# Performance work log

Measured on AMD Instinct MI355X. Metric: run time of the kernel, lower is better.

The kernel has to match this reference:

```python
import jax, jax.numpy as jnp
import numpy as np

B, L, D, H, S = 2, 2048, 1024, 16, 4
Dh = D // H
EPS = 1e-5


def setup_inputs() -> dict:
    key = jax.random.key(0)
    ks = jax.random.split(key, 12)
    sc = 0.02
    w = lambda k, shape: (jax.random.normal(k, shape, jnp.float32) * sc)
    M = 2 * S  # number of MHA blocks / dense linears
    inp = {
        "response": jax.random.normal(ks[0], (B, L, D), jnp.float32),
        "mask": jnp.broadcast_to(jnp.tril(jnp.ones((L, L), bool)), (B, L, L)),
        "Wq": w(ks[1], (M, D, D)), "bq": w(ks[2], (M, D)),
        "Wk": w(ks[3], (M, D, D)), "bk": w(ks[4], (M, D)),
        "Wv": w(ks[5], (M, D, D)), "bv": w(ks[6], (M, D)),
        "Wo": w(ks[7], (M, D, D)), "bo": w(ks[8], (M, D)),
        "Wd": w(ks[9], (M, D, D)), "bd": w(ks[10], (M, D)),
    }
    return inp


def _ln(x):
    # fresh LayerNorm(d) with default weight=1, bias=0, eps=1e-5
    m = jnp.mean(x, axis=-1, keepdims=True)
    v = jnp.mean((x - m) ** 2, axis=-1, keepdims=True)
    return (x - m) * jax.lax.rsqrt(v + EPS)


def _linear(x, W, b):
    # torch Linear: x @ W.T + b
    return jnp.einsum('bld,od->blo', x, W) + b


def _mha(x, i, mask, Wq, bq, Wk, bk, Wv, bv, Wo, bo):
    # self-attention: q = k = v = x
    split = lambda y: y.reshape(B, L, H, Dh).transpose(0, 2, 1, 3)  # (B,H,L,Dh)
    q = split(_linear(x, Wq[i], bq[i]))
    k = split(_linear(x, Wk[i], bk[i]))
    v = split(_linear(x, Wv[i], bv[i]))
    scores = jnp.einsum('bhqd,bhkd->bhqk', q, k) / jnp.sqrt(jnp.float32(Dh))
    if mask is not None:
        scores = jnp.where(mask[:, None, :, :], scores, -jnp.inf)
    p = jnp.nan_to_num(jax.nn.softmax(scores, axis=-1))
    o = jnp.einsum('bhqk,bhkd->bhqd', p, v).transpose(0, 2, 1, 3).reshape(B, L, D)
    return _linear(o, Wo[i], bo[i])


def reference(response, mask, Wq, bq, Wk, bk, Wv, bv, Wo, bo, Wd, bd):
    x = response
    for i in range(S):
        # masked self-attention + residual + LN
        x = _ln(x + _mha(x, 2 * i, mask, Wq, bq, Wk, bk, Wv, bv, Wo, bo))
        # encoder-attention sublayer (encMem is None -> unmasked self-attention)
        x = _ln(x + _mha(x, 2 * i + 1, None, Wq, bq, Wk, bk, Wv, bv, Wo, bo))
        # dense: linear[2i](LeakyReLU(linear[2i+1](x)))
        h = jax.nn.leaky_relu(_linear(x, Wd[2 * i + 1], bd[2 * i + 1]), negative_slope=0.01)
        h = _linear(h, Wd[2 * i], bd[2 * i])
        x = _ln(x + h)
    return x
```

## Files before the change

kernel.cpp:

```cpp
#include <hip/hip_runtime.h>
#include <stdint.h>
#include <stddef.h>

typedef __attribute__((ext_vector_type(8))) _Float16 f16x8;
typedef __attribute__((ext_vector_type(4))) _Float16 f16x4;
typedef __attribute__((ext_vector_type(4))) float    f32x4;

#define NB 2
#define NL 2048
#define ND 1024
#define NH 16
#define NROWS (NB*NL)

__device__ __forceinline__ void async16(void* lds, const void* g) {
  __builtin_amdgcn_global_load_lds(
      (const __attribute__((address_space(1))) void*)g,
      (__attribute__((address_space(3))) void*)lds, 16, 0, 0);
}

struct CvtArgs { const float* in[5]; _Float16* out[5]; };

__global__ __launch_bounds__(256) void cvt_all(CvtArgs a, int n4)
{
  const float* in  = a.in[blockIdx.z];
  _Float16*   out  = a.out[blockIdx.z];
  for (int i = blockIdx.x * blockDim.x + threadIdx.x; i < n4;
       i += gridDim.x * blockDim.x) {
    float4 v = ((const float4*)in)[i];
    f16x4 o = {(_Float16)v.x, (_Float16)v.y, (_Float16)v.z, (_Float16)v.w};
    ((f16x4*)out)[i] = o;
  }
}

__global__ __launch_bounds__(256) void init_x(
    const float* __restrict__ r, float* __restrict__ x,
    _Float16* __restrict__ xh, int n4)
{
  for (int i = blockIdx.x * blockDim.x + threadIdx.x; i < n4;
       i += gridDim.x * blockDim.x) {
    float4 v = ((const float4*)r)[i];
    ((float4*)x)[i] = v;
    f16x4 o = {(_Float16)v.x, (_Float16)v.y, (_Float16)v.z, (_Float16)v.w};
    ((f16x4*)xh)[i] = o;
  }
}

struct GArgs {
  const _Float16* A;
  const _Float16* B[3];
  const float*    bias[3];
  void*           out[3];
  int             mode[3];
};

__global__ __launch_bounds__(256, 2) void gemm_bt(GArgs ga)
{
  __shared__ _Float16 As[2][128 * 64];
  __shared__ _Float16 Bs[2][128 * 64];
  const int tid = threadIdx.x;
  const int w = tid >> 6, l = tid & 63;
  const int ql = l & 15, g = l >> 4;
  const int widx = blockIdx.x >> 3;
  const _Float16* Bw  = ga.B[widx];
  const float*   bias = ga.bias[widx];
  void*          outp = ga.out[widx];
  const int      mode = ga.mode[widx];
  const int brow = blockIdx.y * 128;
  const int bcol = (blockIdx.x & 7) * 128;
  const int wm = w >> 1, wn = w & 1;
  f32x4 acc[4][4] = {};

  const int srow = w * 32 + (l >> 3);
  const int scol = ((l & 7) ^ (l >> 3)) << 3;
  const _Float16* Ag = ga.A + (size_t)(brow + srow) * ND + scol;
  const _Float16* Bg = Bw   + (size_t)(bcol + srow) * ND + scol;

#define STAGE(buf, k0_)                                                  \
  {                                                                      \
    _Float16* AsW = &As[buf][w * 2048];                                  \
    _Float16* BsW = &Bs[buf][w * 2048];                                  \
    _Pragma("unroll")                                                    \
    for (int i = 0; i < 4; ++i) {                                        \
      async16(AsW + i * 512, Ag + (size_t)i * 8 * ND + (k0_));           \
      async16(BsW + i * 512, Bg + (size_t)i * 8 * ND + (k0_));           \
    }                                                                    \
  }

  STAGE(0, 0);
  for (int k0 = 0; k0 < ND; k0 += 64) {
    const int cur = (k0 >> 6) & 1;
    if (k0 + 64 < ND) {
      STAGE(cur ^ 1, k0 + 64);
      asm volatile("s_waitcnt vmcnt(8)" ::: "memory");
    } else {
      asm volatile("s_waitcnt vmcnt(0)" ::: "memory");
    }
    __builtin_amdgcn_s_barrier();
#pragma unroll
    for (int ks = 0; ks < 64; ks += 32) {
      const int cx = (ks + g * 8) ^ ((ql & 7) << 3);
      f16x8 af[4], bf[4];
#pragma unroll
      for (int mi = 0; mi < 4; ++mi)
        af[mi] = *(const f16x8*)&As[cur][(wm * 64 + mi * 16 + ql) * 64 + cx];
#pragma unroll
      for (int nj = 0; nj < 4; ++nj)
        bf[nj] = *(const f16x8*)&Bs[cur][(wn * 64 + nj * 16 + ql) * 64 + cx];
#pragma unroll
      for (int mi = 0; mi < 4; ++mi)
#pragma unroll
        for (int nj = 0; nj < 4; ++nj)
          acc[mi][nj] = __builtin_amdgcn_mfma_f32_16x16x32_f16(
              af[mi], bf[nj], acc[mi][nj], 0, 0, 0);
    }
    asm volatile("s_waitcnt lgkmcnt(0)" ::: "memory");
    __builtin_amdgcn_s_barrier();
  }
#undef STAGE

  const int colb = bcol + wn * 64;
  const int rowb = brow + wm * 64 + g * 4;
  if (mode == 3) {
    _Float16* vt = (_Float16*)outp;
    const int bb = rowb >> 11;
#pragma unroll
    for (int nj = 0; nj < 4; ++nj) {
      const int col = colb + nj * 16 + ql;
      const float bv = bias[col];
      const int hh = col >> 6, d = col & 63;
      _Float16* vrow = vt + ((size_t)((bb * NH + hh) * 64 + d)) * NL;
#pragma unroll
      for (int mi = 0; mi < 4; ++mi) {
        const int krow = (rowb + mi * 16) & (NL - 1);
        f16x4 o;
#pragma unroll
        for (int r = 0; r < 4; ++r) o[r] = (_Float16)(acc[mi][nj][r] + bv);
        *(f16x4*)(vrow + krow) = o;
      }
    }
  } else {
    _Float16* oh = (_Float16*)outp;
#pragma unroll
    for (int nj = 0; nj < 4; ++nj) {
      const int col = colb + nj * 16 + ql;
      const float bv = bias[col];
#pragma unroll
      for (int mi = 0; mi < 4; ++mi) {
#pragma unroll
        for (int r = 0; r < 4; ++r) {
          float v = acc[mi][nj][r] + bv;
          if (mode == 2) v = v > 0.f ? v : 0.01f * v;
          oh[(size_t)(rowb + mi * 16 + r) * ND + col] = (_Float16)v;
        }
      }
    }
  }
}

template<bool CAUSAL>
__global__ __launch_bounds__(512) void attn_fwd(
    const _Float16* __restrict__ Q, const _Float16* __restrict__ K,
    const _Float16* __restrict__ Vt, _Float16* __restrict__ O)
{
  __shared__ _Float16 kv[2][2][64 * 64];
  __shared__ unsigned int pls[8][16 * 34];
  const int tid = threadIdx.x;
  const int w = tid >> 6, l = tid & 63;
  const int ql = l & 15, g = l >> 4;
  const int h = blockIdx.y, b = blockIdx.z;
  const int qt = (CAUSAL && b) ? (NL / 128 - 1 - blockIdx.x) : blockIdx.x;
  const int qrow = qt * 128 + w * 16 + ql;

  const _Float16* Qp = Q + (size_t)(b * NL + qrow) * ND + h * 64 + g * 8;
  const f16x8 bq0 = *(const f16x8*)Qp;
  const f16x8 bq1 = *(const f16x8*)(Qp + 32);

  const int srow = w * 8 + (l >> 3);
  const int scol = ((l & 7) ^ (l >> 3)) << 3;
  const _Float16* Kg = K  + ((size_t)(b * NL) + srow) * ND + h * 64 + scol;
  const _Float16* Vg = Vt + ((size_t)((b * NH + h) * 64 + srow)) * NL + scol;

  const int msk  = (ql & 7) << 3;
  const int offA = ql * 64 + ((     g * 8) ^ msk);
  const int offB = ql * 64 + ((32 + g * 8) ^ msk);

  unsigned int* pw = &pls[w][0];
  f32x4 ot[4] = {};
  float s_run = 0.f;
  const int ntiles = CAUSAL ? (qt * 2 + 2) : (NL / 64);
  const float SCL = 0.125f * 1.44269504089f;
  const float M2  = 4.0f * 1.44269504089f;

  async16(&kv[0][0][w * 512], Kg);
  async16(&kv[0][1][w * 512], Vg);

  for (int kt = 0; kt < ntiles; ++kt) {
    const int nb = kt & 1;
    const size_t nk0 = (size_t)((kt + 1 < ntiles) ? kt + 1 : kt) * 64;
    async16(&kv[nb ^ 1][0][w * 512], Kg + nk0 * ND);
    async16(&kv[nb ^ 1][1][w * 512], Vg + nk0);
    asm volatile("s_waitcnt vmcnt(2)" ::: "memory");
    __builtin_amdgcn_s_barrier();

    const _Float16* kb = &kv[nb][0][0];
    const _Float16* vb = &kv[nb][1][0];
    const int k0 = kt * 64;
    f32x4 st[4] = {};
#pragma unroll
    for (int sub = 0; sub < 4; ++sub) {
      const f16x8 a0 = *(const f16x8*)&kb[sub * 1024 + offA];
      const f16x8 a1 = *(const f16x8*)&kb[sub * 1024 + offB];
      st[sub] = __builtin_amdgcn_mfma_f32_16x16x32_f16(a0, bq0, st[sub], 0, 0, 0);
      st[sub] = __builtin_amdgcn_mfma_f32_16x16x32_f16(a1, bq1, st[sub], 0, 0, 0);
    }
    float ps = 0.f;
    float pv[16];
#pragma unroll
    for (int sub = 0; sub < 4; ++sub)
#pragma unroll
      for (int r = 0; r < 4; ++r) {
        float p = exp2f(__builtin_fmaf(st[sub][r], SCL, -M2));
        if (CAUSAL && (k0 + sub * 16 + g * 4 + r) > qrow) p = 0.f;
        pv[sub * 4 + r] = p;
        ps += p;
      }
#pragma unroll
    for (int sub = 0; sub < 4; ++sub) {
      uint2 uu;
      uu.x = __builtin_bit_cast(unsigned int,
                __builtin_amdgcn_cvt_pkrtz(pv[sub * 4 + 0], pv[sub * 4 + 1]));
      uu.y = __builtin_bit_cast(unsigned int,
                __builtin_amdgcn_cvt_pkrtz(pv[sub * 4 + 2], pv[sub * 4 + 3]));
      *(uint2*)&pw[(sub * 4 + g) * 34 + 2 * ql] = uu;
    }
    ps += __shfl_xor(ps, 16);
    ps += __shfl_xor(ps, 32);
    s_run += ps;

#pragma unroll
    for (int hh = 0; hh < 2; ++hh) {
      uint2 lo = *(const uint2*)&pw[(hh * 8 + 2 * g    ) * 34 + 2 * ql];
      uint2 hi = *(const uint2*)&pw[(hh * 8 + 2 * g + 1) * 34 + 2 * ql];
      uint4 ui; ui.x = lo.x; ui.y = lo.y; ui.z = hi.x; ui.w = hi.y;
      const f16x8 pf = __builtin_bit_cast(f16x8, ui);
      const int voff = hh ? offB : offA;
#pragma unroll
      for (int dt = 0; dt < 4; ++dt) {
        const f16x8 vf = *(const f16x8*)&vb[dt * 1024 + voff];
        ot[dt] = __builtin_amdgcn_mfma_f32_16x16x32_f16(vf, pf, ot[dt], 0, 0, 0);
      }
    }
    asm volatile("s_waitcnt lgkmcnt(0)" ::: "memory");
    __builtin_amdgcn_s_barrier();
  }

  const float inv = 1.f / s_run;
#pragma unroll
  for (int dt = 0; dt < 4; ++dt) {
    f16x4 o;
#pragma unroll
    for (int r = 0; r < 4; ++r) o[r] = (_Float16)(ot[dt][r] * inv);
    *(f16x4*)(O + (size_t)(b * NL + qrow) * ND + h * 64 + dt * 16 + g * 4) = o;
  }
}

__global__ __launch_bounds__(256) void resid_ln(
    const float* __restrict__ x, const _Float16* __restrict__ dlt,
    float* __restrict__ xo, _Float16* __restrict__ xh)
{
  const int row = blockIdx.x, tid = threadIdx.x;
  const float4 xv = ((const float4*)(x + (size_t)row * ND))[tid];
  const f16x4 dv = ((const f16x4*)(dlt + (size_t)row * ND))[tid];
  const float a = xv.x + (float)dv[0], b = xv.y + (float)dv[1];
  const float c = xv.z + (float)dv[2], d = xv.w + (float)dv[3];
  float s = a + b + c + d;
  float ss = a * a + b * b + c * c + d * d;
#pragma unroll
  for (int m = 1; m < 64; m <<= 1) {
    s  += __shfl_xor(s, m);
    ss += __shfl_xor(ss, m);
  }
  __shared__ float red[8];
  if ((tid & 63) == 0) { red[tid >> 6] = s; red[4 + (tid >> 6)] = ss; }
  __syncthreads();
  const float S  = red[0] + red[1] + red[2] + red[3];
  const float SS = red[4] + red[5] + red[6] + red[7];
  const float mean = S * (1.0f / ND);
  const float var  = SS * (1.0f / ND) - mean * mean;
  const float rstd = rsqrtf(fmaxf(var, 0.f) + 1e-5f);
  float4 y;
  y.x = (a - mean) * rstd; y.y = (b - mean) * rstd;
  y.z = (c - mean) * rstd; y.w = (d - mean) * rstd;
  ((float4*)(xo + (size_t)row * ND))[tid] = y;
  f16x4 yh = {(_Float16)y.x, (_Float16)y.y, (_Float16)y.z, (_Float16)y.w};
  ((f16x4*)(xh + (size_t)row * ND))[tid] = yh;
}

extern "C" void kernel_launch(void* const* d_in, const int* in_sizes, int n_in,
                              void* d_out, int out_size, void* d_ws, size_t ws_size,
                              hipStream_t stream)
{
  (void)in_sizes; (void)n_in; (void)out_size; (void)ws_size;
  const float* response = (const float*)d_in[0];
  const float* Wq = (const float*)d_in[2];
  const float* bq = (const float*)d_in[3];
  const float* Wk = (const float*)d_in[4];
  const float* bk = (const float*)d_in[5];
  const float* Wv = (const float*)d_in[6];
  const float* bv = (const float*)d_in[7];
  const float* Wo = (const float*)d_in[8];
  const float* bo = (const float*)d_in[9];
  const float* Wd = (const float*)d_in[10];
  const float* bd = (const float*)d_in[11];
  float* x = (float*)d_out;

  const size_t MB = 1024 * 1024;
  char* p = (char*)d_ws;
  _Float16* Wq_h = (_Float16*)(p + 0 * MB);
  _Float16* Wk_h = (_Float16*)(p + 16 * MB);
  _Float16* Wv_h = (_Float16*)(p + 32 * MB);
  _Float16* Wo_h = (_Float16*)(p + 48 * MB);
  _Float16* Wd_h = (_Float16*)(p + 64 * MB);
  _Float16* xh   = (_Float16*)(p + 80 * MB);
  _Float16* Qh   = (_Float16*)(p + 88 * MB);
  _Float16* Kh   = (_Float16*)(p + 96 * MB);
  _Float16* Vth  = (_Float16*)(p + 104 * MB);
  _Float16* Oh   = (_Float16*)(p + 112 * MB);
  _Float16* h1   = Qh;
  _Float16* tmp  = (_Float16*)(p + 96 * MB);

  const int wn4 = 8 * 1024 * 1024 / 4;
  CvtArgs ca = { { Wq, Wk, Wv, Wo, Wd }, { Wq_h, Wk_h, Wv_h, Wo_h, Wd_h } };
  cvt_all<<<dim3(256, 1, 5), 256, 0, stream>>>(ca, wn4);
  init_x<<<1024, 256, 0, stream>>>(response, x, xh, NROWS * ND / 4);

  const dim3 g3(24, NROWS / 128);
  const dim3 g1(8, NROWS / 128);
  const dim3 agrid(NL / 128, NH, NB);

  for (int i = 0; i < 4; ++i) {
    for (int sub = 0; sub < 2; ++sub) {
      const int m = 2 * i + sub;
      const size_t wo = (size_t)m * MB;
      const size_t bf = (size_t)m * 1024;
      GArgs qkv = { xh,
                    { Wq_h + wo, Wk_h + wo, Wv_h + wo },
                    { bq + bf, bk + bf, bv + bf },
                    { Qh, Kh, Vth }, { 0, 0, 3 } };
      gemm_bt<<<g3, 256, 0, stream>>>(qkv);
      if (sub == 0) attn_fwd<true ><<<agrid, 512, 0, stream>>>(Qh, Kh, Vth, Oh);
      else          attn_fwd<false><<<agrid, 512, 0, stream>>>(Qh, Kh, Vth, Oh);
      GArgs oprj = { Oh,
                     { Wo_h + wo, nullptr, nullptr },
                     { bo + bf, nullptr, nullptr },
                     { tmp, nullptr, nullptr }, { 0, 0, 0 } };
      gemm_bt<<<g1, 256, 0, stream>>>(oprj);
      resid_ln<<<NROWS, 256, 0, stream>>>(x, tmp, x, xh);
    }
    const size_t w1 = (size_t)(2 * i + 1) * MB, b1 = (size_t)(2 * i + 1) * 1024;
    const size_t w0 = (size_t)(2 * i) * MB,     b0 = (size_t)(2 * i) * 1024;
    GArgs f1 = { xh,
                 { Wd_h + w1, nullptr, nullptr },
                 { bd + b1, nullptr, nullptr },
                 { h1, nullptr, nullptr }, { 2, 0, 0 } };
    gemm_bt<<<g1, 256, 0, stream>>>(f1);
    GArgs f2 = { h1,
                 { Wd_h + w0, nullptr, nullptr },
                 { bd + b0, nullptr, nullptr },
                 { tmp, nullptr, nullptr }, { 0, 0, 0 } };
    gemm_bt<<<g1, 256, 0, stream>>>(f2);
    resid_ln<<<NROWS, 256, 0, stream>>>(x, tmp, x, xh);
  }
}
```

Baseline: 1.320 ms.

## Split-K the output and second FFN GEMMs; give attention waves two query fragments

The O-projection and second dense GEMM now split K into two halves across blockIdx.z and write fp16 partials to two buffers. The residual-LayerNorm kernel sums both partials, which doubles the block count for 1024-wide GEMMs that previously launched only 256 blocks. Separately, the attention kernel drops from 8 waves of 16 query rows to 4 waves of 32 rows each, so every K/V fragment loaded from LDS feeds two query tiles, with launch bounds set for three blocks per CU. The cost is extra partial-sum traffic, fp16 rounding of each partial, and more registers per attention wave.

```diff
diff --git a/kernel.cpp b/kernel.cpp
--- a/kernel.cpp
+++ b/kernel.cpp
@@ -51,6 +51,7 @@
   const float*    bias[3];
   void*           out[3];
   int             mode[3];
+  int             ksplit;
 };
 
 __global__ __launch_bounds__(256, 2) void gemm_bt(GArgs ga)
@@ -60,11 +61,15 @@
   const int tid = threadIdx.x;
   const int w = tid >> 6, l = tid & 63;
   const int ql = l & 15, g = l >> 4;
-  const int widx = blockIdx.x >> 3;
+  const int z = blockIdx.z;
+  const int widx = ga.ksplit ? 0 : (blockIdx.x >> 3);
   const _Float16* Bw  = ga.B[widx];
   const float*   bias = ga.bias[widx];
-  void*          outp = ga.out[widx];
+  void*          outp = ga.ksplit ? ga.out[z] : ga.out[widx];
   const int      mode = ga.mode[widx];
+  const int kbeg = ga.ksplit ? z * (ND / 2) : 0;
+  const int kend = ga.ksplit ? kbeg + ND / 2 : ND;
+  const bool dobias = (!ga.ksplit) || (z == 0);
   const int brow = blockIdx.y * 128;
   const int bcol = (blockIdx.x & 7) * 128;
   const int wm = w >> 1, wn = w & 1;
@@ -86,10 +91,10 @@
     }                                                                    \
   }
 
-  STAGE(0, 0);
-  for (int k0 = 0; k0 < ND; k0 += 64) {
-    const int cur = (k0 >> 6) & 1;
-    if (k0 + 64 < ND) {
+  STAGE(0, kbeg);
+  for (int k0 = kbeg; k0 < kend; k0 += 64) {
+    const int cur = ((k0 - kbeg) >> 6) & 1;
+    if (k0 + 64 < kend) {
       STAGE(cur ^ 1, k0 + 64);
       asm volatile("s_waitcnt vmcnt(8)" ::: "memory");
     } else {
@@ -143,7 +148,7 @@
 #pragma unroll
     for (int nj = 0; nj < 4; ++nj) {
       const int col = colb + nj * 16 + ql;
-      const float bv = bias[col];
+      const float bv = dobias ? bias[col] : 0.f;
 #pragma unroll
       for (int mi = 0; mi < 4; ++mi) {
 #pragma unroll
@@ -158,24 +163,29 @@
 }
 
 template<bool CAUSAL>
-__global__ __launch_bounds__(512) void attn_fwd(
+__global__ __launch_bounds__(256, 3) void attn_fwd(
     const _Float16* __restrict__ Q, const _Float16* __restrict__ K,
     const _Float16* __restrict__ Vt, _Float16* __restrict__ O)
 {
   __shared__ _Float16 kv[2][2][64 * 64];
-  __shared__ unsigned int pls[8][16 * 34];
+  __shared__ unsigned int pls[4][2][16 * 34];
   const int tid = threadIdx.x;
   const int w = tid >> 6, l = tid & 63;
   const int ql = l & 15, g = l >> 4;
   const int h = blockIdx.y, b = blockIdx.z;
-  const int qt = (CAUSAL && b) ? (NL / 128 - 1 - blockIdx.x) : blockIdx.x;
-  const int qrow = qt * 128 + w * 16 + ql;
-
-  const _Float16* Qp = Q + (size_t)(b * NL + qrow) * ND + h * 64 + g * 8;
-  const f16x8 bq0 = *(const f16x8*)Qp;
-  const f16x8 bq1 = *(const f16x8*)(Qp + 32);
-
-  const int srow = w * 8 + (l >> 3);
+  const int qt = (CAUSAL && b) ? (NL / 128 - 1 - (int)blockIdx.x) : blockIdx.x;
+
+  f16x8 bq[2][2];
+  int qrow[2];
+#pragma unroll
+  for (int f = 0; f < 2; ++f) {
+    qrow[f] = qt * 128 + w * 32 + f * 16 + ql;
+    const _Float16* Qp = Q + (size_t)(b * NL + qrow[f]) * ND + h * 64 + g * 8;
+    bq[f][0] = *(const f16x8*)Qp;
+    bq[f][1] = *(const f16x8*)(Qp + 32);
+  }
+
+  const int srow = w * 16 + (l >> 3);
   const int scol = ((l & 7) ^ (l >> 3)) << 3;
   const _Float16* Kg = K  + ((size_t)(b * NL) + srow) * ND + h * 64 + scol;
   const _Float16* Vg = Vt + ((size_t)((b * NH + h) * 64 + srow)) * NL + scol;
@@ -184,95 +194,114 @@
   const int offA = ql * 64 + ((     g * 8) ^ msk);
   const int offB = ql * 64 + ((32 + g * 8) ^ msk);
 
-  unsigned int* pw = &pls[w][0];
-  f32x4 ot[4] = {};
-  float s_run = 0.f;
+  f32x4 ot[2][4] = {};
+  float s_run[2] = {0.f, 0.f};
   const int ntiles = CAUSAL ? (qt * 2 + 2) : (NL / 64);
   const float SCL = 0.125f * 1.44269504089f;
   const float M2  = 4.0f * 1.44269504089f;
 
-  async16(&kv[0][0][w * 512], Kg);
-  async16(&kv[0][1][w * 512], Vg);
+  async16(&kv[0][0][w * 1024      ], Kg);
+  async16(&kv[0][0][w * 1024 + 512], Kg + (size_t)8 * ND);
+  async16(&kv[0][1][w * 1024      ], Vg);
+  async16(&kv[0][1][w * 1024 + 512], Vg + (size_t)8 * NL);
 
   for (int kt = 0; kt < ntiles; ++kt) {
     const int nb = kt & 1;
     const size_t nk0 = (size_t)((kt + 1 < ntiles) ? kt + 1 : kt) * 64;
-    async16(&kv[nb ^ 1][0][w * 512], Kg + nk0 * ND);
-    async16(&kv[nb ^ 1][1][w * 512], Vg + nk0);
-    asm volatile("s_waitcnt vmcnt(2)" ::: "memory");
+    async16(&kv[nb ^ 1][0][w * 1024      ], Kg + nk0 * ND);
+    async16(&kv[nb ^ 1][0][w * 1024 + 512], Kg + nk0 * ND + (size_t)8 * ND);
+    async16(&kv[nb ^ 1][1][w * 1024      ], Vg + nk0);
+    async16(&kv[nb ^ 1][1][w * 1024 + 512], Vg + nk0 + (size_t)8 * NL);
+    asm volatile("s_waitcnt vmcnt(4)" ::: "memory");
     __builtin_amdgcn_s_barrier();
 
     const _Float16* kb = &kv[nb][0][0];
     const _Float16* vb = &kv[nb][1][0];
     const int k0 = kt * 64;
-    f32x4 st[4] = {};
-#pragma unroll
-    for (int sub = 0; sub < 4; ++sub) {
-      const f16x8 a0 = *(const f16x8*)&kb[sub * 1024 + offA];
-      const f16x8 a1 = *(const f16x8*)&kb[sub * 1024 + offB];
-      st[sub] = __builtin_amdgcn_mfma_f32_16x16x32_f16(a0, bq0, st[sub], 0, 0, 0);
-      st[sub] = __builtin_amdgcn_mfma_f32_16x16x32_f16(a1, bq1, st[sub], 0, 0, 0);
-    }
-    float ps = 0.f;
-    float pv[16];
-#pragma unroll
-    for (int sub = 0; sub < 4; ++sub)
-#pragma unroll
-      for (int r = 0; r < 4; ++r) {
-        float p = exp2f(__builtin_fmaf(st[sub][r], SCL, -M2));
-        if (CAUSAL && (k0 + sub * 16 + g * 4 + r) > qrow) p = 0.f;
-        pv[sub * 4 + r] = p;
-        ps += p;
-      }
-#pragma unroll
-    for (int sub = 0; sub < 4; ++sub) {
-      uint2 uu;
-      uu.x = __builtin_bit_cast(unsigned int,
-                __builtin_amdgcn_cvt_pkrtz(pv[sub * 4 + 0], pv[sub * 4 + 1]));
-      uu.y = __builtin_bit_cast(unsigned int,
-                __builtin_amdgcn_cvt_pkrtz(pv[sub * 4 + 2], pv[sub * 4 + 3]));
-      *(uint2*)&pw[(sub * 4 + g) * 34 + 2 * ql] = uu;
-    }
-    ps += __shfl_xor(ps, 16);
-    ps += __shfl_xor(ps, 32);
-    s_run += ps;
+
+#pragma unroll
+    for (int f = 0; f < 2; ++f) {
+      f32x4 st[4] = {};
+#pragma unroll
+      for (int sub = 0; sub < 4; ++sub) {
+        const f16x8 a0 = *(const f16x8*)&kb[sub * 1024 + offA];
+        const f16x8 a1 = *(const f16x8*)&kb[sub * 1024 + offB];
+        st[sub] = __builtin_amdgcn_mfma_f32_16x16x32_f16(a0, bq[f][0], st[sub], 0, 0, 0);
+        st[sub] = __builtin_amdgcn_mfma_f32_16x16x32_f16(a1, bq[f][1], st[sub], 0, 0, 0);
+      }
+      float ps = 0.f;
+      float pv[16];
+#pragma unroll
+      for (int sub = 0; sub < 4; ++sub)
+#pragma unroll
+        for (int r = 0; r < 4; ++r) {
+          float p = exp2f(__builtin_fmaf(st[sub][r], SCL, -M2));
+          if (CAUSAL && (k0 + sub * 16 + g * 4 + r) > qrow[f]) p = 0.f;
+          pv[sub * 4 + r] = p;
+          ps += p;
+        }
+#pragma unroll
+      for (int sub = 0; sub < 4; ++sub) {
+        uint2 uu;
+        uu.x = __builtin_bit_cast(unsigned int,
+                  __builtin_amdgcn_cvt_pkrtz(pv[sub * 4 + 0], pv[sub * 4 + 1]));
+        uu.y = __builtin_bit_cast(unsigned int,
+                  __builtin_amdgcn_cvt_pkrtz(pv[sub * 4 + 2], pv[sub * 4 + 3]));
+        *(uint2*)&pls[w][f][(sub * 4 + g) * 34 + 2 * ql] = uu;
+      }
+      ps += __shfl_xor(ps, 16);
+      ps += __shfl_xor(ps, 32);
+      s_run[f] += ps;
+    }
 
 #pragma unroll
     for (int hh = 0; hh < 2; ++hh) {
-      uint2 lo = *(const uint2*)&pw[(hh * 8 + 2 * g    ) * 34 + 2 * ql];
-      uint2 hi = *(const uint2*)&pw[(hh * 8 + 2 * g + 1) * 34 + 2 * ql];
-      uint4 ui; ui.x = lo.x; ui.y = lo.y; ui.z = hi.x; ui.w = hi.y;
-      const f16x8 pf = __builtin_bit_cast(f16x8, ui);
+      f16x8 pf[2];
+#pragma unroll
+      for (int f = 0; f < 2; ++f) {
+        uint2 lo = *(const uint2*)&pls[w][f][(hh * 8 + 2 * g    ) * 34 + 2 * ql];
+        uint2 hi = *(const uint2*)&pls[w][f][(hh * 8 + 2 * g + 1) * 34 + 2 * ql];
+        uint4 ui; ui.x = lo.x; ui.y = lo.y; ui.z = hi.x; ui.w = hi.y;
+        pf[f] = __builtin_bit_cast(f16x8, ui);
+      }
       const int voff = hh ? offB : offA;
 #pragma unroll
       for (int dt = 0; dt < 4; ++dt) {
         const f16x8 vf = *(const f16x8*)&vb[dt * 1024 + voff];
-        ot[dt] = __builtin_amdgcn_mfma_f32_16x16x32_f16(vf, pf, ot[dt], 0, 0, 0);
+        ot[0][dt] = __builtin_amdgcn_mfma_f32_16x16x32_f16(vf, pf[0], ot[0][dt], 0, 0, 0);
+        ot[1][dt] = __builtin_amdgcn_mfma_f32_16x16x32_f16(vf, pf[1], ot[1][dt], 0, 0, 0);
       }
     }
     asm volatile("s_waitcnt lgkmcnt(0)" ::: "memory");
     __builtin_amdgcn_s_barrier();
   }
 
-  const float inv = 1.f / s_run;
-#pragma unroll
-  for (int dt = 0; dt < 4; ++dt) {
-    f16x4 o;
-#pragma unroll
-    for (int r = 0; r < 4; ++r) o[r] = (_Float16)(ot[dt][r] * inv);
-    *(f16x4*)(O + (size_t)(b * NL + qrow) * ND + h * 64 + dt * 16 + g * 4) = o;
+#pragma unroll
+  for (int f = 0; f < 2; ++f) {
+    const float inv = 1.f / s_run[f];
+#pragma unroll
+    for (int dt = 0; dt < 4; ++dt) {
+      f16x4 o;
+#pragma unroll
+      for (int r = 0; r < 4; ++r) o[r] = (_Float16)(ot[f][dt][r] * inv);
+      *(f16x4*)(O + (size_t)(b * NL + qrow[f]) * ND + h * 64 + dt * 16 + g * 4) = o;
+    }
   }
 }
 
 __global__ __launch_bounds__(256) void resid_ln(
-    const float* __restrict__ x, const _Float16* __restrict__ dlt,
+    const float* __restrict__ x, const _Float16* __restrict__ d0,
+    const _Float16* __restrict__ d1,
     float* __restrict__ xo, _Float16* __restrict__ xh)
 {
   const int row = blockIdx.x, tid = threadIdx.x;
   const float4 xv = ((const float4*)(x + (size_t)row * ND))[tid];
-  const f16x4 dv = ((const f16x4*)(dlt + (size_t)row * ND))[tid];
-  const float a = xv.x + (float)dv[0], b = xv.y + (float)dv[1];
-  const float c = xv.z + (float)dv[2], d = xv.w + (float)dv[3];
+  const f16x4 v0 = ((const f16x4*)(d0 + (size_t)row * ND))[tid];
+  const f16x4 v1 = ((const f16x4*)(d1 + (size_t)row * ND))[tid];
+  const float a = xv.x + (float)v0[0] + (float)v1[0];
+  const float b = xv.y + (float)v0[1] + (float)v1[1];
+  const float c = xv.z + (float)v0[2] + (float)v1[2];
+  const float d = xv.w + (float)v0[3] + (float)v1[3];
   float s = a + b + c + d;
   float ss = a * a + b * b + c * c + d * d;
 #pragma unroll
@@ -327,15 +356,17 @@
   _Float16* Vth  = (_Float16*)(p + 104 * MB);
   _Float16* Oh   = (_Float16*)(p + 112 * MB);
   _Float16* h1   = Qh;
-  _Float16* tmp  = (_Float16*)(p + 96 * MB);
+  _Float16* t0   = (_Float16*)(p + 96 * MB);
+  _Float16* t1   = (_Float16*)(p + 104 * MB);
 
   const int wn4 = 8 * 1024 * 1024 / 4;
   CvtArgs ca = { { Wq, Wk, Wv, Wo, Wd }, { Wq_h, Wk_h, Wv_h, Wo_h, Wd_h } };
   cvt_all<<<dim3(256, 1, 5), 256, 0, stream>>>(ca, wn4);
   init_x<<<1024, 256, 0, stream>>>(response, x, xh, NROWS * ND / 4);
 
-  const dim3 g3(24, NROWS / 128);
-  const dim3 g1(8, NROWS / 128);
+  const dim3 g3(24, NROWS / 128, 1);
+  const dim3 gs(8, NROWS / 128, 2);
+  const dim3 gf(8, NROWS / 128, 1);
   const dim3 agrid(NL / 128, NH, NB);
 
   for (int i = 0; i < 4; ++i) {
@@ -346,29 +377,29 @@
       GArgs qkv = { xh,
                     { Wq_h + wo, Wk_h + wo, Wv_h + wo },
                     { bq + bf, bk + bf, bv + bf },
-                    { Qh, Kh, Vth }, { 0, 0, 3 } };
+                    { Qh, Kh, Vth }, { 0, 0, 3 }, 0 };
       gemm_bt<<<g3, 256, 0, stream>>>(qkv);
-      if (sub == 0) attn_fwd<true ><<<agrid, 512, 0, stream>>>(Qh, Kh, Vth, Oh);
-      else          attn_fwd<false><<<agrid, 512, 0, stream>>>(Qh, Kh, Vth, Oh);
+      if (sub == 0) attn_fwd<true ><<<agrid, 256, 0, stream>>>(Qh, Kh, Vth, Oh);
+      else          attn_fwd<false><<<agrid, 256, 0, stream>>>(Qh, Kh, Vth, Oh);
       GArgs oprj = { Oh,
                      { Wo_h + wo, nullptr, nullptr },
                      { bo + bf, nullptr, nullptr },
-                     { tmp, nullptr, nullptr }, { 0, 0, 0 } };
-      gemm_bt<<<g1, 256, 0, stream>>>(oprj);
-      resid_ln<<<NROWS, 256, 0, stream>>>(x, tmp, x, xh);
+                     { t0, t1, nullptr }, { 0, 0, 0 }, 1 };
+      gemm_bt<<<gs, 256, 0, stream>>>(oprj);
+      resid_ln<<<NROWS, 256, 0, stream>>>(x, t0, t1, x, xh);
     }
     const size_t w1 = (size_t)(2 * i + 1) * MB, b1 = (size_t)(2 * i + 1) * 1024;
     const size_t w0 = (size_t)(2 * i) * MB,     b0 = (size_t)(2 * i) * 1024;
     GArgs f1 = { xh,
                  { Wd_h + w1, nullptr, nullptr },
                  { bd + b1, nullptr, nullptr },
-                 { h1, nullptr, nullptr }, { 2, 0, 0 } };
-    gemm_bt<<<g1, 256, 0, stream>>>(f1);
+                 { h1, nullptr, nullptr }, { 2, 0, 0 }, 0 };
+    gemm_bt<<<gf, 256, 0, stream>>>(f1);
     GArgs f2 = { h1,
                  { Wd_h + w0, nullptr, nullptr },
                  { bd + b0, nullptr, nullptr },
-                 { tmp, nullptr, nullptr }, { 0, 0, 0 } };
-    gemm_bt<<<g1, 256, 0, stream>>>(f2);
-    resid_ln<<<NROWS, 256, 0, stream>>>(x, tmp, x, xh);
-  }
-}
+                 { t0, t1, nullptr }, { 0, 0, 0 }, 1 };
+    gemm_bt<<<gs, 256, 0, stream>>>(f2);
+    resid_ln<<<NROWS, 256, 0, stream>>>(x, t0, t1, x, xh);
+  }
+}
```

New measurement: 1.354 ms. 1.03x slower.
